# Optimization experiments

Hardware: AMD Instinct MI355X
Metric: run time of the kernel (lower is better)

## Reference

```python
import jax, jax.numpy as jnp
import numpy as np

SEQ_LEN = 4096
EMBED_DIM = 2048
NUM_HEADS = 16
HEAD_DIM = EMBED_DIM // NUM_HEADS


def setup_inputs() -> dict:
    key = jax.random.key(0)
    k1, k2, k3 = jax.random.split(key, 3)
    x = jax.random.normal(k1, (SEQ_LEN, EMBED_DIM), dtype=jnp.float32)
    # Dense-layer params (lecun-normal-ish scaling for stability)
    W_qkv = jax.random.normal(k2, (EMBED_DIM, 3 * EMBED_DIM), dtype=jnp.float32) / np.sqrt(EMBED_DIM)
    b_qkv = jnp.zeros((3 * EMBED_DIM,), dtype=jnp.float32)
    W_out = jax.random.normal(k3, (EMBED_DIM, EMBED_DIM), dtype=jnp.float32) / np.sqrt(EMBED_DIM)
    b_out = jnp.zeros((EMBED_DIM,), dtype=jnp.float32)
    return {"x": x, "W_qkv": W_qkv, "b_qkv": b_qkv, "W_out": W_out, "b_out": b_out}


def reference(x, W_qkv, b_qkv, W_out, b_out):
    seq_len = x.shape[0]
    qkv = x @ W_qkv + b_qkv                       # (S, 3E)
    qkv = qkv.reshape(seq_len, 3, NUM_HEADS, HEAD_DIM)
    q, k, v = qkv[:, 0], qkv[:, 1], qkv[:, 2]     # each (S, H, D)
    scale = 1.0 / jnp.sqrt(jnp.float32(HEAD_DIM))
    # NOTE: faithful to source -- contracts over BOTH heads and head_dim,
    # producing a single (S, S) attention matrix shared across heads.
    attn = jnp.einsum('thd,shd->ts', q, k) * scale
    causal = jnp.triu(jnp.ones((seq_len, seq_len), dtype=bool), k=1)
    attn = jnp.where(causal, -jnp.inf, attn)
    attn = jax.nn.softmax(attn, axis=-1)
    out = jnp.einsum('ts,shd->thd', attn, v)      # (S, H, D)
    out = out.reshape(seq_len, EMBED_DIM)
    return out @ W_out + b_out
```

## Files before the change

kernel.cpp:

```cpp
#include <hip/hip_runtime.h>
#include <cstdint>
#include <cstddef>

#define SEQLEN 4096
#define EMBED  2048
#define NH     16
#define HD     128
#define N3     6144
#define SCALE  0.08838834764831845f
#define MBIAS  25.0f
#define LB3    12288
#define LB4    12288
#define LB1    8192

typedef __attribute__((ext_vector_type(8))) short bf16x8;
typedef __attribute__((ext_vector_type(4))) float f32x4;
typedef unsigned short u16;

#define MFMA(a, b, c) __builtin_amdgcn_mfma_f32_16x16x32_bf16((a), (b), (c), 0, 0, 0)

__device__ inline u16 f2bf(float f) {
  uint32_t u = __float_as_uint(f);
  u += 0x7FFF + ((u >> 16) & 1);
  return (u16)(u >> 16);
}

__device__ inline float bf2f(u16 u) {
  return __uint_as_float(((uint32_t)u) << 16);
}

__device__ inline void gload_lds16(const u16* g, u16* l) {
  __builtin_amdgcn_global_load_lds((const __attribute__((address_space(1))) void*)g,
                                   (__attribute__((address_space(3))) void*)l, 16, 0, 0);
}

__device__ __forceinline__ void stage3(const u16* a0, const u16* a1, const u16* b0,
                                       u16* base, int w, int lane) {
  gload_lds16(a0, base + w * 512 + lane * 8);
  gload_lds16(a1, base + 4096 + w * 512 + lane * 8);
  gload_lds16(b0, base + 8192 + w * 512 + lane * 8);
}

__device__ __forceinline__ void mm256x128(const u16* gA, size_t sA, const u16* gB, size_t sB,
                                          int NT, u16* lds, f32x4 (&acc)[4][4]) {
  int tid = threadIdx.x;
  int w = tid >> 6, lane = tid & 63;
  int g = lane >> 4, lr = lane & 15;
  int wm = w >> 1, wn = w & 1;
  int arow = (w << 4) + (lane >> 2);
  int cb = (((lane & 3) ^ (arow & 3)) << 3);
  const u16* a0 = gA + (size_t)arow * sA + cb;
  const u16* a1 = a0 + (size_t)128 * sA;
  const u16* b0 = gB + (size_t)arow * sB + cb;
  int gx = ((g ^ (lr & 3)) << 3);
  int aoff = ((wm << 6) + lr) * 32 + gx;
  int boff = 8192 + ((wn << 6) + lr) * 32 + gx;
  stage3(a0, a1, b0, lds, w, lane);
  stage3(a0 + 32, a1 + 32, b0 + 32, lds + LB3, w, lane);
  asm volatile("s_waitcnt vmcnt(3)" ::: "memory");
  __builtin_amdgcn_s_barrier();
  for (int t = 0; t < NT; ++t) {
    u16* base = lds + (t % 3) * LB3;
    bf16x8 af[4], bfr[4];
    #pragma unroll
    for (int m = 0; m < 4; m++) af[m] = *(const bf16x8*)(base + aoff + m * 512);
    #pragma unroll
    for (int n = 0; n < 4; n++) bfr[n] = *(const bf16x8*)(base + boff + n * 512);
    if (t + 2 < NT) {
      int kt = (t + 2) << 5;
      stage3(a0 + kt, a1 + kt, b0 + kt, lds + ((t + 2) % 3) * LB3, w, lane);
    }
    __builtin_amdgcn_s_setprio(1);
    #pragma unroll
    for (int m = 0; m < 4; m++)
      #pragma unroll
      for (int n = 0; n < 4; n++)
        acc[m][n] = MFMA(af[m], bfr[n], acc[m][n]);
    __builtin_amdgcn_s_setprio(0);
    if (t + 1 < NT) {
      if (t + 2 < NT) asm volatile("s_waitcnt vmcnt(3)" ::: "memory");
      else            asm volatile("s_waitcnt vmcnt(0)" ::: "memory");
      __builtin_amdgcn_s_barrier();
    }
  }
  asm volatile("" ::: "memory");
}

__device__ __forceinline__ void stage6(const u16* a0, const u16* a1, const u16* a2, const u16* a3,
                                       const u16* b0, const u16* b1, u16* base, int w, int lane) {
  gload_lds16(a0, base + w * 512 + lane * 8);
  gload_lds16(a1, base + 2048 + w * 512 + lane * 8);
  gload_lds16(a2, base + 4096 + w * 512 + lane * 8);
  gload_lds16(a3, base + 6144 + w * 512 + lane * 8);
  gload_lds16(b0, base + 8192 + w * 512 + lane * 8);
  gload_lds16(b1, base + 10240 + w * 512 + lane * 8);
}

__device__ __forceinline__ void mm256x128w4(const u16* gA, size_t sA, const u16* gB, size_t sB,
                                            int NT, u16* lds, f32x4 (&acc)[8][4]) {
  int tid = threadIdx.x;
  int w = tid >> 6, lane = tid & 63;
  int g = lane >> 4, lr = lane & 15;
  int wm = w >> 1, wn = w & 1;
  int arow = (w << 4) + (lane >> 2);
  int cb = (((lane & 3) ^ (arow & 3)) << 3);
  const u16* a0 = gA + (size_t)arow * sA + cb;
  const u16* a1 = a0 + (size_t)64 * sA;
  const u16* a2 = a0 + (size_t)128 * sA;
  const u16* a3 = a0 + (size_t)192 * sA;
  const u16* b0 = gB + (size_t)arow * sB + cb;
  const u16* b1 = b0 + (size_t)64 * sB;
  int gx = ((g ^ (lr & 3)) << 3);
  int aoff = ((wm << 7) + lr) * 32 + gx;
  int boff = 8192 + ((wn << 6) + lr) * 32 + gx;
  stage6(a0, a1, a2, a3, b0, b1, lds, w, lane);
  stage6(a0 + 32, a1 + 32, a2 + 32, a3 + 32, b0 + 32, b1 + 32, lds + LB4, w, lane);
  asm volatile("s_waitcnt vmcnt(6)" ::: "memory");
  __builtin_amdgcn_s_barrier();
  for (int t = 0; t < NT; ++t) {
    u16* base = lds + (t % 3) * LB4;
    bf16x8 af[8], bfr[4];
    #pragma unroll
    for (int m = 0; m < 8; m++) af[m] = *(const bf16x8*)(base + aoff + m * 512);
    #pragma unroll
    for (int n = 0; n < 4; n++) bfr[n] = *(const bf16x8*)(base + boff + n * 512);
    if (t + 2 < NT) {
      int kt = (t + 2) << 5;
      stage6(a0 + kt, a1 + kt, a2 + kt, a3 + kt, b0 + kt, b1 + kt,
             lds + ((t + 2) % 3) * LB4, w, lane);
    }
    __builtin_amdgcn_s_setprio(1);
    #pragma unroll
    for (int m = 0; m < 8; m++)
      #pragma unroll
      for (int n = 0; n < 4; n++)
        acc[m][n] = MFMA(af[m], bfr[n], acc[m][n]);
    __builtin_amdgcn_s_setprio(0);
    if (t + 1 < NT) {
      if (t + 2 < NT) asm volatile("s_waitcnt vmcnt(6)" ::: "memory");
      else            asm volatile("s_waitcnt vmcnt(0)" ::: "memory");
      __builtin_amdgcn_s_barrier();
    }
  }
  asm volatile("" ::: "memory");
}

__device__ __forceinline__ void stage2h(const u16* a0, const u16* b0, u16* base, int w, int lane) {
  gload_lds16(a0, base + w * 512 + lane * 8);
  gload_lds16(b0, base + 4096 + w * 512 + lane * 8);
}

__device__ __forceinline__ void mm128x128(const u16* gA, size_t sA, const u16* gB, size_t sB,
                                          int NT, u16* lds, f32x4 (&acc)[4][2]) {
  int tid = threadIdx.x;
  int w = tid >> 6, lane = tid & 63;
  int g = lane >> 4, lr = lane & 15;
  int wm = w >> 2, wn = w & 3;
  int srow = lane >> 2;
  int cb = (((lane & 3) ^ (srow & 3)) << 3);
  const u16* a0 = gA + (size_t)((w << 4) + srow) * sA + cb;
  const u16* b0 = gB + (size_t)((w << 4) + srow) * sB + cb;
  int gx = ((g ^ (lr & 3)) << 3);
  int aoff = ((wm << 6) + lr) * 32 + gx;
  int boff = 4096 + ((wn << 5) + lr) * 32 + gx;
  stage2h(a0, b0, lds, w, lane);
  stage2h(a0 + 32, b0 + 32, lds + LB1, w, lane);
  asm volatile("s_waitcnt vmcnt(2)" ::: "memory");
  __builtin_amdgcn_s_barrier();
  for (int t = 0; t < NT; ++t) {
    u16* base = lds + (t % 3) * LB1;
    bf16x8 af[4], bfr[2];
    #pragma unroll
    for (int m = 0; m < 4; m++) af[m] = *(const bf16x8*)(base + aoff + m * 512);
    #pragma unroll
    for (int n = 0; n < 2; n++) bfr[n] = *(const bf16x8*)(base + boff + n * 512);
    if (t + 2 < NT) {
      int kt = (t + 2) << 5;
      stage2h(a0 + kt, b0 + kt, lds + ((t + 2) % 3) * LB1, w, lane);
    }
    __builtin_amdgcn_s_setprio(1);
    #pragma unroll
    for (int m = 0; m < 4; m++)
      #pragma unroll
      for (int n = 0; n < 2; n++)
        acc[m][n] = MFMA(af[m], bfr[n], acc[m][n]);
    __builtin_amdgcn_s_setprio(0);
    if (t + 1 < NT) {
      if (t + 2 < NT) asm volatile("s_waitcnt vmcnt(2)" ::: "memory");
      else            asm volatile("s_waitcnt vmcnt(0)" ::: "memory");
      __builtin_amdgcn_s_barrier();
    }
  }
  asm volatile("" ::: "memory");
}

__global__ __launch_bounds__(256) void conv_f32_bf16(const float* __restrict__ in,
                                                     u16* __restrict__ out, int n) {
  int i = (blockIdx.x * 256 + threadIdx.x) * 4;
  if (i >= n) return;
  float4 v = *(const float4*)(in + i);
  ushort4 o;
  o.x = f2bf(v.x); o.y = f2bf(v.y); o.z = f2bf(v.z); o.w = f2bf(v.w);
  *(ushort4*)(out + i) = o;
}

__global__ __launch_bounds__(256) void transpose_conv(const float* __restrict__ in,
                                                      u16* __restrict__ out, int R, int C) {
  __shared__ float t[32][33];
  int c0 = blockIdx.x * 32, r0 = blockIdx.y * 32;
  int tx = threadIdx.x, ty = threadIdx.y;
  #pragma unroll
  for (int i = ty; i < 32; i += 8)
    t[i][tx] = in[(size_t)(r0 + i) * C + c0 + tx];
  __syncthreads();
  #pragma unroll
  for (int i = ty; i < 32; i += 8)
    out[(size_t)(c0 + i) * R + r0 + tx] = f2bf(t[tx][i]);
}

__global__ __launch_bounds__(256) void vtrans(const u16* __restrict__ qkv, u16* __restrict__ vT) {
  __shared__ u16 t[32][33];
  int c0 = blockIdx.x * 32, t0 = blockIdx.y * 32;
  int tx = threadIdx.x, ty = threadIdx.y;
  #pragma unroll
  for (int i = ty; i < 32; i += 8)
    t[i][tx] = qkv[(size_t)(t0 + i) * N3 + 2 * EMBED + c0 + tx];
  __syncthreads();
  #pragma unroll
  for (int i = ty; i < 32; i += 8)
    vT[(size_t)(c0 + i) * SEQLEN + t0 + tx] = t[tx][i];
}

__global__ __launch_bounds__(256, 2) void gemm_bt4(const u16* __restrict__ A, const u16* __restrict__ Bt,
                                                   const float* __restrict__ bias,
                                                   u16* __restrict__ Cb, int N, int K) {
  __shared__ __align__(16) u16 lds[3 * LB4];
  int bm = blockIdx.x, bn = blockIdx.y;
  f32x4 acc[8][4] = {};
  mm256x128w4(A + (size_t)(bm * 256) * K, K, Bt + (size_t)(bn * 128) * K, K, K >> 5, lds, acc);
  int tid = threadIdx.x;
  int w = tid >> 6, lane = tid & 63, g = lane >> 4, lr = lane & 15;
  int wm = w >> 1, wn = w & 1;
  int r0 = bm * 256 + wm * 128, c0 = bn * 128 + wn * 64;
  #pragma unroll
  for (int n = 0; n < 4; n++) {
    int c = c0 + n * 16 + lr;
    float bv = bias[c];
    #pragma unroll
    for (int m = 0; m < 8; m++)
      #pragma unroll
      for (int j = 0; j < 4; j++) {
        int r = r0 + m * 16 + g * 4 + j;
        Cb[(size_t)r * N + c] = f2bf(acc[m][n][j] + bv);
      }
  }
}

__global__ __launch_bounds__(512, 4) void gemm_bt2(const u16* __restrict__ A, const u16* __restrict__ Bt,
                                                   const float* __restrict__ bias,
                                                   float* __restrict__ Cf, int N, int K) {
  __shared__ __align__(16) u16 lds[3 * LB3];
  int bm = blockIdx.x, bn = blockIdx.y;
  f32x4 acc[4][4] = {};
  mm256x128(A + (size_t)(bm * 256) * K, K, Bt + (size_t)(bn * 128) * K, K, K >> 5, lds, acc);
  int tid = threadIdx.x;
  int w = tid >> 6, lane = tid & 63, g = lane >> 4, lr = lane & 15;
  int wm = w >> 1, wn = w & 1;
  int r0 = bm * 256 + wm * 64, c0 = bn * 128 + wn * 64;
  #pragma unroll
  for (int n = 0; n < 4; n++) {
    int c = c0 + n * 16 + lr;
    float bv = bias[c];
    #pragma unroll
    for (int m = 0; m < 4; m++)
      #pragma unroll
      for (int j = 0; j < 4; j++) {
        int r = r0 + m * 16 + g * 4 + j;
        Cf[(size_t)r * N + c] = acc[m][n][j] + bv;
      }
  }
}

__global__ __launch_bounds__(256, 2) void sgemm_p4(const u16* __restrict__ qkv,
                                                   u16* __restrict__ P,
                                                   float* __restrict__ Lpart) {
  int by = blockIdx.x, bx = blockIdx.y;
  int r0g = by * 256, c0g = bx * 128;
  if (c0g > r0g + 255) return;
  __shared__ __align__(16) u16 lds[3 * LB4];
  f32x4 acc[8][4] = {};
  mm256x128w4(qkv + (size_t)r0g * N3, N3, qkv + (size_t)c0g * N3 + EMBED, N3, EMBED >> 5, lds, acc);
  int tid = threadIdx.x;
  int w = tid >> 6, lane = tid & 63, g = lane >> 4, lr = lane & 15;
  int wm = w >> 1, wn = w & 1;
  int r0 = r0g + wm * 128, c0 = c0g + wn * 64;
  int slot = bx * 2 + wn;
  #pragma unroll
  for (int m = 0; m < 8; m++)
    #pragma unroll
    for (int j = 0; j < 4; j++) {
      int r = r0 + m * 16 + g * 4 + j;
      float psv = 0.f;
      #pragma unroll
      for (int n = 0; n < 4; n++) {
        int c = c0 + n * 16 + lr;
        float p = (c <= r) ? __expf(fmaf(acc[m][n][j], SCALE, -MBIAS)) : 0.f;
        P[(size_t)r * SEQLEN + c] = f2bf(p);
        psv += p;
      }
      psv += __shfl_xor(psv, 1);  psv += __shfl_xor(psv, 2);
      psv += __shfl_xor(psv, 4);  psv += __shfl_xor(psv, 8);
      if (lr == 0) Lpart[(size_t)r * 64 + slot] = psv;
    }
}

__global__ __launch_bounds__(256) void psum_small(const float* __restrict__ Lpart,
                                                  float* __restrict__ L) {
  int wave = threadIdx.x >> 6, lane = threadIdx.x & 63;
  int r = blockIdx.x * 4 + wave;
  float s = Lpart[(size_t)r * 64 + lane];
  s += __shfl_xor(s, 1);  s += __shfl_xor(s, 2);  s += __shfl_xor(s, 4);
  s += __shfl_xor(s, 8);  s += __shfl_xor(s, 16); s += __shfl_xor(s, 32);
  if (lane == 0) L[r] = s;
}

__global__ __launch_bounds__(512, 4) void pv_gemm3(const u16* __restrict__ P,
                                                   const u16* __restrict__ vT,
                                                   const float* __restrict__ L,
                                                   u16* __restrict__ O) {
  __shared__ __align__(16) u16 lds[3 * LB1];
  int pp = blockIdx.x, bx = blockIdx.y;
  int tid = threadIdx.x;
  int w = tid >> 6, lane = tid & 63, g = lane >> 4, lr = lane & 15;
  int wm = w >> 2, wn = w & 3;
  int c0g = bx * 128;
  #pragma unroll
  for (int pass = 0; pass < 2; pass++) {
    int rt = pass ? pp : (31 - pp);
    int r0g = rt * 128;
    int NT = (r0g + 128) >> 5;
    f32x4 acc[4][2] = {};
    mm128x128(P + (size_t)r0g * SEQLEN, SEQLEN, vT + (size_t)c0g * SEQLEN, SEQLEN, NT, lds, acc);
    int r0 = r0g + wm * 64, c0 = c0g + wn * 32;
    #pragma unroll
    for (int m = 0; m < 4; m++) {
      float invl[4];
      #pragma unroll
      for (int j = 0; j < 4; j++)
        invl[j] = 1.f / L[r0 + m * 16 + g * 4 + j];
      #pragma unroll
      for (int n = 0; n < 2; n++) {
        int c = c0 + n * 16 + lr;
        #pragma unroll
        for (int j = 0; j < 4; j++) {
          int r = r0 + m * 16 + g * 4 + j;
          O[(size_t)r * EMBED + c] = f2bf(acc[m][n][j] * invl[j]);
        }
      }
    }
    __syncthreads();
  }
}

extern "C" void kernel_launch(void* const* d_in, const int* in_sizes, int n_in,
                              void* d_out, int out_size, void* d_ws, size_t ws_size,
                              hipStream_t stream) {
  const float* x     = (const float*)d_in[0];
  const float* W_qkv = (const float*)d_in[1];
  const float* b_qkv = (const float*)d_in[2];
  const float* W_out = (const float*)d_in[3];
  const float* b_out = (const float*)d_in[4];
  float* out = (float*)d_out;

  u16* xb    = (u16*)d_ws;
  u16* qkvb  = xb + (size_t)SEQLEN * EMBED;
  u16* Pbuf  = qkvb + (size_t)SEQLEN * N3;
  u16* vT    = Pbuf + (size_t)SEQLEN * SEQLEN;
  float* Lbuf = (float*)(vT + (size_t)EMBED * SEQLEN);
  u16* attb  = xb;
  u16* WqkvT = Pbuf;
  u16* WoutT = Pbuf;
  float* Lpart = (float*)xb;

  conv_f32_bf16<<<SEQLEN * EMBED / 1024, 256, 0, stream>>>(x, xb, SEQLEN * EMBED);
  transpose_conv<<<dim3(N3 / 32, EMBED / 32), dim3(32, 8), 0, stream>>>(W_qkv, WqkvT, EMBED, N3);
  gemm_bt4<<<dim3(SEQLEN / 256, N3 / 128), 256, 0, stream>>>(xb, WqkvT, b_qkv, qkvb, N3, EMBED);
  vtrans<<<dim3(EMBED / 32, SEQLEN / 32), dim3(32, 8), 0, stream>>>(qkvb, vT);
  hipMemsetAsync(Lpart, 0, (size_t)SEQLEN * 64 * sizeof(float), stream);
  sgemm_p4<<<dim3(SEQLEN / 256, SEQLEN / 128), 256, 0, stream>>>(qkvb, Pbuf, Lpart);
  psum_small<<<SEQLEN / 4, 256, 0, stream>>>(Lpart, Lbuf);
  pv_gemm3<<<dim3(16, EMBED / 128), 512, 0, stream>>>(Pbuf, vT, Lbuf, attb);
  transpose_conv<<<dim3(EMBED / 32, EMBED / 32), dim3(32, 8), 0, stream>>>(W_out, WoutT, EMBED, EMBED);
  gemm_bt2<<<dim3(SEQLEN / 256, EMBED / 128), 512, 0, stream>>>(attb, WoutT, b_out, out, EMBED, EMBED);
}
```

Before: 316.5 us.

## Use 256x256 QKV GEMM tile and fuse V transpose into its epilogue

Replaces the 256x128 QKV projection GEMM (4 waves) with a 256x256 tile kernel using 8 waves and larger triple-buffered LDS stages. Blocks covering the V columns write their output directly in transposed layout into vT, which removes the separate vtrans kernel and its extra read and write of V. The larger tile raises data reuse per block but cuts the grid to 384 blocks at one block per CU and uses 96KB of LDS, so latency hiding and the final wave could get worse.

```diff
diff --git a/kernel.cpp b/kernel.cpp
--- a/kernel.cpp
+++ b/kernel.cpp
@@ -11,6 +11,7 @@
 #define MBIAS  25.0f
 #define LB3    12288
 #define LB4    12288
+#define LB5    16384
 #define LB1    8192
 
 typedef __attribute__((ext_vector_type(8))) short bf16x8;
@@ -79,6 +80,60 @@
     __builtin_amdgcn_s_setprio(0);
     if (t + 1 < NT) {
       if (t + 2 < NT) asm volatile("s_waitcnt vmcnt(3)" ::: "memory");
+      else            asm volatile("s_waitcnt vmcnt(0)" ::: "memory");
+      __builtin_amdgcn_s_barrier();
+    }
+  }
+  asm volatile("" ::: "memory");
+}
+
+__device__ __forceinline__ void stage4(const u16* a0, const u16* a1, const u16* b0, const u16* b1,
+                                       u16* base, int w, int lane) {
+  gload_lds16(a0, base + w * 512 + lane * 8);
+  gload_lds16(a1, base + 4096 + w * 512 + lane * 8);
+  gload_lds16(b0, base + 8192 + w * 512 + lane * 8);
+  gload_lds16(b1, base + 12288 + w * 512 + lane * 8);
+}
+
+__device__ __forceinline__ void mm256x256(const u16* gA, size_t sA, const u16* gB, size_t sB,
+                                          int NT, u16* lds, f32x4 (&acc)[8][4]) {
+  int tid = threadIdx.x;
+  int w = tid >> 6, lane = tid & 63;
+  int g = lane >> 4, lr = lane & 15;
+  int wm = w >> 2, wn = w & 3;
+  int arow = (w << 4) + (lane >> 2);
+  int cb = (((lane & 3) ^ (arow & 3)) << 3);
+  const u16* a0 = gA + (size_t)arow * sA + cb;
+  const u16* a1 = a0 + (size_t)128 * sA;
+  const u16* b0 = gB + (size_t)arow * sB + cb;
+  const u16* b1 = b0 + (size_t)128 * sB;
+  int gx = ((g ^ (lr & 3)) << 3);
+  int aoff = wm * 4096 + lr * 32 + gx;
+  int boff = 8192 + wn * 2048 + lr * 32 + gx;
+  stage4(a0, a1, b0, b1, lds, w, lane);
+  stage4(a0 + 32, a1 + 32, b0 + 32, b1 + 32, lds + LB5, w, lane);
+  asm volatile("s_waitcnt vmcnt(4)" ::: "memory");
+  __builtin_amdgcn_s_barrier();
+  for (int t = 0; t < NT; ++t) {
+    u16* base = lds + (t % 3) * LB5;
+    bf16x8 af[8], bfr[4];
+    #pragma unroll
+    for (int m = 0; m < 8; m++) af[m] = *(const bf16x8*)(base + aoff + m * 512);
+    #pragma unroll
+    for (int n = 0; n < 4; n++) bfr[n] = *(const bf16x8*)(base + boff + n * 512);
+    if (t + 2 < NT) {
+      int kt = (t + 2) << 5;
+      stage4(a0 + kt, a1 + kt, b0 + kt, b1 + kt, lds + ((t + 2) % 3) * LB5, w, lane);
+    }
+    __builtin_amdgcn_s_setprio(1);
+    #pragma unroll
+    for (int m = 0; m < 8; m++)
+      #pragma unroll
+      for (int n = 0; n < 4; n++)
+        acc[m][n] = MFMA(af[m], bfr[n], acc[m][n]);
+    __builtin_amdgcn_s_setprio(0);
+    if (t + 1 < NT) {
+      if (t + 2 < NT) asm volatile("s_waitcnt vmcnt(4)" ::: "memory");
       else            asm volatile("s_waitcnt vmcnt(0)" ::: "memory");
       __builtin_amdgcn_s_barrier();
     }
@@ -218,41 +273,47 @@
     out[(size_t)(c0 + i) * R + r0 + tx] = f2bf(t[tx][i]);
 }
 
-__global__ __launch_bounds__(256) void vtrans(const u16* __restrict__ qkv, u16* __restrict__ vT) {
-  __shared__ u16 t[32][33];
-  int c0 = blockIdx.x * 32, t0 = blockIdx.y * 32;
-  int tx = threadIdx.x, ty = threadIdx.y;
-  #pragma unroll
-  for (int i = ty; i < 32; i += 8)
-    t[i][tx] = qkv[(size_t)(t0 + i) * N3 + 2 * EMBED + c0 + tx];
-  __syncthreads();
-  #pragma unroll
-  for (int i = ty; i < 32; i += 8)
-    vT[(size_t)(c0 + i) * SEQLEN + t0 + tx] = t[tx][i];
-}
-
-__global__ __launch_bounds__(256, 2) void gemm_bt4(const u16* __restrict__ A, const u16* __restrict__ Bt,
-                                                   const float* __restrict__ bias,
-                                                   u16* __restrict__ Cb, int N, int K) {
-  __shared__ __align__(16) u16 lds[3 * LB4];
+__global__ __launch_bounds__(512, 1) void gemm_qkv256(const u16* __restrict__ A, const u16* __restrict__ Bt,
+                                                      const float* __restrict__ bias,
+                                                      u16* __restrict__ Cb, u16* __restrict__ vT,
+                                                      int N, int K) {
+  __shared__ __align__(16) u16 lds[3 * LB5];
   int bm = blockIdx.x, bn = blockIdx.y;
   f32x4 acc[8][4] = {};
-  mm256x128w4(A + (size_t)(bm * 256) * K, K, Bt + (size_t)(bn * 128) * K, K, K >> 5, lds, acc);
+  mm256x256(A + (size_t)(bm * 256) * K, K, Bt + (size_t)(bn * 256) * K, K, K >> 5, lds, acc);
   int tid = threadIdx.x;
   int w = tid >> 6, lane = tid & 63, g = lane >> 4, lr = lane & 15;
-  int wm = w >> 1, wn = w & 1;
-  int r0 = bm * 256 + wm * 128, c0 = bn * 128 + wn * 64;
-  #pragma unroll
-  for (int n = 0; n < 4; n++) {
-    int c = c0 + n * 16 + lr;
-    float bv = bias[c];
-    #pragma unroll
-    for (int m = 0; m < 8; m++)
-      #pragma unroll
-      for (int j = 0; j < 4; j++) {
-        int r = r0 + m * 16 + g * 4 + j;
-        Cb[(size_t)r * N + c] = f2bf(acc[m][n][j] + bv);
+  int wm = w >> 2, wn = w & 3;
+  int r0 = bm * 256 + wm * 128, c0 = bn * 256 + wn * 64;
+  if (bn < 16) {
+    #pragma unroll
+    for (int n = 0; n < 4; n++) {
+      int c = c0 + n * 16 + lr;
+      float bv = bias[c];
+      #pragma unroll
+      for (int m = 0; m < 8; m++)
+        #pragma unroll
+        for (int j = 0; j < 4; j++) {
+          int r = r0 + m * 16 + g * 4 + j;
+          Cb[(size_t)r * N + c] = f2bf(acc[m][n][j] + bv);
+        }
+    }
+  } else {
+    #pragma unroll
+    for (int n = 0; n < 4; n++) {
+      int c = c0 + n * 16 + lr;
+      float bv = bias[c];
+      int vrow = c - 2 * EMBED;
+      #pragma unroll
+      for (int m = 0; m < 8; m++) {
+        ushort4 o;
+        o.x = f2bf(acc[m][n][0] + bv);
+        o.y = f2bf(acc[m][n][1] + bv);
+        o.z = f2bf(acc[m][n][2] + bv);
+        o.w = f2bf(acc[m][n][3] + bv);
+        *(ushort4*)(vT + (size_t)vrow * SEQLEN + r0 + m * 16 + g * 4) = o;
       }
+    }
   }
 }
 
@@ -384,8 +445,8 @@
 
   conv_f32_bf16<<<SEQLEN * EMBED / 1024, 256, 0, stream>>>(x, xb, SEQLEN * EMBED);
   transpose_conv<<<dim3(N3 / 32, EMBED / 32), dim3(32, 8), 0, stream>>>(W_qkv, WqkvT, EMBED, N3);
-  gemm_bt4<<<dim3(SEQLEN / 256, N3 / 128), 256, 0, stream>>>(xb, WqkvT, b_qkv, qkvb, N3, EMBED);
-  vtrans<<<dim3(EMBED / 32, SEQLEN / 32), dim3(32, 8), 0, stream>>>(qkvb, vT);
+  gemm_qkv256<<<dim3(SEQLEN / 256, N3 / 256), 512, 0, stream>>>(xb, WqkvT, b_qkv, qkvb, vT,
+                                                                N3, EMBED);
   hipMemsetAsync(Lpart, 0, (size_t)SEQLEN * 64 * sizeof(float), stream);
   sgemm_p4<<<dim3(SEQLEN / 256, SEQLEN / 128), 256, 0, stream>>>(qkvb, Pbuf, Lpart);
   psum_small<<<SEQLEN / 4, 256, 0, stream>>>(Lpart, Lbuf);
```

After: 323.6 us. 1.02x slower.
